# Optimization experiments

Hardware: AMD Instinct MI355X
Metric: run time of the kernel (lower is better)

## Reference

```python
import jax, jax.numpy as jnp
import numpy as np
from jax import lax

D_MODEL = 1024
SEQ_LEN = 8192
ORDER = 2
BATCH = 2

def setup_inputs() -> dict:
    key = jax.random.key(0)
    ks = jax.random.split(key, 16)
    s = 0.02
    return {
        'x': jax.random.normal(ks[0], (BATCH, SEQ_LEN, D_MODEL), jnp.float32),
        'in_proj_w': jax.random.normal(ks[1], (D_MODEL, D_MODEL * (ORDER + 1)), jnp.float32) * s,
        'in_proj_b': jax.random.normal(ks[2], (D_MODEL * (ORDER + 1),), jnp.float32) * s,
        'short_w': jax.random.normal(ks[3], (D_MODEL, 1, 3), jnp.float32) * 0.5,
        'short_b': jax.random.normal(ks[4], (D_MODEL,), jnp.float32) * s,
        'fw1': jax.random.normal(ks[5], (1, 64), jnp.float32) * 0.5,
        'fb1': jax.random.normal(ks[6], (64,), jnp.float32) * s,
        'fw2': jax.random.normal(ks[7], (64, 128), jnp.float32) * 0.1,
        'fb2': jax.random.normal(ks[8], (128,), jnp.float32) * s,
        'fw3': jax.random.normal(ks[9], (128, D_MODEL * ORDER), jnp.float32) * 0.05,
        'fb3': jax.random.normal(ks[10], (D_MODEL * ORDER,), jnp.float32) * s,
        'out_w': jax.random.normal(ks[11], (D_MODEL, D_MODEL), jnp.float32) * s,
        'out_b': jax.random.normal(ks[12], (D_MODEL,), jnp.float32) * s,
    }

def _hyena_fwd(x, in_proj_w, in_proj_b, short_w, short_b,
               fw1, fb1, fw2, fb2, fw3, fb3, out_w, out_b):
    B, L, C = x.shape
    # in_proj: (B, L, C*(order+1)) -> split into v and order gating branches
    proj = (x @ in_proj_w + in_proj_b).reshape(B, L, C, ORDER + 1)
    v = proj[..., 0]                                   # (B, L, C)
    x_branches = [proj[..., i] for i in range(1, ORDER + 1)]
    # depthwise short conv (kernel 3, same padding), torch Conv1d groups=C
    vc = v.transpose(0, 2, 1)                          # (B, C, L)
    vc = lax.conv_general_dilated(vc, short_w, window_strides=(1,),
                                  padding=((1, 1),), feature_group_count=C,
                                  dimension_numbers=('NCH', 'OIH', 'NCH'))
    v = (vc + short_b[None, :, None]).transpose(0, 2, 1)  # (B, L, C)
    # implicit filter: MLP over normalized positions (exact GELU as in torch)
    pos = jnp.linspace(0.0, 1.0, L, dtype=x.dtype)[:, None]   # (L, 1)
    h = jax.nn.gelu(pos @ fw1 + fb1, approximate=False)
    h = jax.nn.gelu(h @ fw2 + fb2, approximate=False)
    coefs = (h @ fw3 + fb3).reshape(L, C, ORDER)       # (L, C, order)
    # FFT long conv per order; v is constant across the loop (as in source)
    n = 2 * L
    v_fft = jnp.fft.rfft(v, n=n, axis=1)               # (B, L+1, C) complex
    output = v
    for i in range(ORDER):
        h_fft = jnp.fft.rfft(coefs[:, :, i], n=n, axis=0)   # (L+1, C)
        conv = jnp.fft.irfft(v_fft * h_fft[None], n=n, axis=1)[:, :L, :]
        output = x_branches[i] * conv                  # overwrites, as in source
    return output @ out_w + out_b                      # (B, L, C)

def reference(x, in_proj_w, in_proj_b, short_w, short_b,
              fw1, fb1, fw2, fb2, fw3, fb3, out_w, out_b):
    return _hyena_fwd(x, in_proj_w, in_proj_b, short_w, short_b,
                      fw1, fb1, fw2, fb2, fw3, fb3, out_w, out_b)
```

## Files before the change

kernel.cpp:

```cpp
#include <hip/hip_runtime.h>
#include <math.h>


constexpr int Lseq = 8192;
constexpr int Cd   = 1024;
constexpr int BL   = 16384;
constexpr int NF   = 16384;
constexpr int KK   = 1024;
constexpr int FT   = 1024;

constexpr size_t BIG_OFF  = 0;
constexpr size_t COEF_OFF = BIG_OFF + (size_t)2048 * BL;
constexpr size_t W2TH_OFF = COEF_OFF + (size_t)Cd * Lseq;
constexpr size_t W2TL_OFF = W2TH_OFF + (size_t)2048 * 1024 / 2;
constexpr size_t WOTH_OFF = W2TL_OFF + (size_t)2048 * 1024 / 2;
constexpr size_t WOTL_OFF = WOTH_OFF + (size_t)1024 * 1024 / 2;
constexpr size_t B2_OFF   = WOTL_OFF + (size_t)1024 * 1024 / 2;
constexpr size_t WS_FLOATS = B2_OFF + 2048;

using bf16x8 = __attribute__((ext_vector_type(8))) short;
using f32x4  = __attribute__((ext_vector_type(4))) float;

__device__ inline unsigned short f2bf(float f) {
  unsigned u = __float_as_uint(f);
  u += 0x7FFFu + ((u >> 16) & 1u);
  return (unsigned short)(u >> 16);
}
__device__ inline float bf2f(unsigned short h) { return __uint_as_float(((unsigned)h) << 16); }

__device__ inline void gload_lds16(const void* g, void* l) {
  __builtin_amdgcn_global_load_lds((const __attribute__((address_space(1))) unsigned int*)g,
                                   (__attribute__((address_space(3))) unsigned int*)l, 16, 0, 0);
}

__device__ inline float2 cadd(float2 a, float2 b){ return make_float2(a.x+b.x, a.y+b.y); }
__device__ inline float2 csub(float2 a, float2 b){ return make_float2(a.x-b.x, a.y-b.y); }
__device__ inline float2 cmul(float2 a, float2 b){ return make_float2(a.x*b.x - a.y*b.y, a.x*b.y + a.y*b.x); }
__device__ inline float2 cmulc(float2 a, float2 w){ return make_float2(a.x*w.x + a.y*w.y, a.y*w.x - a.x*w.y); }

__device__ inline int PD(int i) { return i + (i >> 4); }

__device__ inline float2 twW(int m) {
  float s, c;
  __sincosf((float)m * -3.8349519697141029e-4f, &s, &c);
  return make_float2(c, s);
}

__device__ inline void fftDIF(float2* __restrict__ z, int t) {
  for (int lq = 12; lq >= 0; lq -= 2) {
    int q    = 1 << lq;
    int twsh = 12 - lq;
    #pragma unroll
    for (int mb = 0; mb < 4; ++mb) {
      int m    = t + mb * FT;
      int tloc = m & (q - 1);
      int g    = m >> lq;
      int base = (g << (lq + 2)) + tloc;
      int i0 = PD(base), i1 = PD(base + q), i2 = PD(base + 2*q), i3 = PD(base + 3*q);
      float2 a = z[i0], b = z[i1], c = z[i2], d = z[i3];
      float2 t0 = cadd(a, c), t1 = csub(a, c);
      float2 t2 = cadd(b, d), t3 = csub(b, d);
      float2 y0 = cadd(t0, t2);
      float2 y2 = csub(t0, t2);
      float2 y1 = make_float2(t1.x + t3.y, t1.y - t3.x);
      float2 y3 = make_float2(t1.x - t3.y, t1.y + t3.x);
      int m1 = tloc << twsh;
      float2 w1 = twW(m1);
      float2 w2 = make_float2(w1.x*w1.x - w1.y*w1.y, 2.f*w1.x*w1.y);
      float2 w3 = cmul(w1, w2);
      z[i0] = y0;
      z[i1] = cmul(y1, w1);
      z[i2] = cmul(y2, w2);
      z[i3] = cmul(y3, w3);
    }
    __syncthreads();
  }
}

__device__ inline void fftDIT(float2* __restrict__ z, int t) {
  for (int lq = 0; lq <= 12; lq += 2) {
    int q    = 1 << lq;
    int twsh = 12 - lq;
    #pragma unroll
    for (int mb = 0; mb < 4; ++mb) {
      int m    = t + mb * FT;
      int tloc = m & (q - 1);
      int g    = m >> lq;
      int base = (g << (lq + 2)) + tloc;
      int i0 = PD(base), i1 = PD(base + q), i2 = PD(base + 2*q), i3 = PD(base + 3*q);
      int m1 = tloc << twsh;
      float2 w1 = twW(m1);
      float2 w2 = make_float2(w1.x*w1.x - w1.y*w1.y, 2.f*w1.x*w1.y);
      float2 w3 = cmul(w1, w2);
      float2 a = z[i0];
      float2 b = cmulc(z[i1], w1);
      float2 c = cmulc(z[i2], w2);
      float2 d = cmulc(z[i3], w3);
      float2 s0 = cadd(a, c), s1 = csub(a, c);
      float2 s2 = cadd(b, d), s3 = csub(b, d);
      z[i0] = cadd(s0, s2);
      z[i1] = make_float2(s1.x - s3.y, s1.y + s3.x);
      z[i2] = csub(s0, s2);
      z[i3] = make_float2(s1.x + s3.y, s1.y - s3.x);
    }
    __syncthreads();
  }
}

__global__ __launch_bounds__(256) void mlp_kernel(const float* __restrict__ fw1, const float* __restrict__ fb1,
                                                  const float* __restrict__ fw2, const float* __restrict__ fb2,
                                                  float* __restrict__ h2) {
  __shared__ float sw2[64 * 128];
  __shared__ float sw1[64], sb1[64], sb2[128];
  int t = threadIdx.x;
  for (int i = t; i < 64 * 128; i += 256) sw2[i] = fw2[i];
  if (t < 64)  { sw1[t] = fw1[t]; sb1[t] = fb1[t]; }
  if (t < 128) sb2[t] = fb2[t];
  __syncthreads();
  int l = blockIdx.x * 256 + t;
  float pos = (float)l / 8191.0f;
  float h1[64];
  #pragma unroll
  for (int j = 0; j < 64; ++j) {
    float xx = pos * sw1[j] + sb1[j];
    h1[j] = 0.5f * xx * (1.0f + erff(xx * 0.7071067811865475f));
  }
  for (int m = 0; m < 128; ++m) {
    float acc = sb2[m];
    #pragma unroll
    for (int j = 0; j < 64; ++j) acc += h1[j] * sw2[j * 128 + m];
    h2[(size_t)l * 128 + m] = 0.5f * acc * (1.0f + erff(acc * 0.7071067811865475f));
  }
}

__global__ __launch_bounds__(256) void gemm_coefs_kernel(const float* __restrict__ H2,
    const float* __restrict__ FW3, const float* __restrict__ FB3,
    float* __restrict__ coefs) {
  __shared__ float As[16 * 72];
  __shared__ float Bs[16 * 72];
  int t  = threadIdx.x;
  int n0 = blockIdx.x * 64;
  int m0 = blockIdx.y * 64;
  int tr = t >> 4, tc = t & 15;
  float acc[4][4] = {};
  int am = t >> 2, ak = (t & 3) * 4;
  int bk = t >> 4, bn = (t & 15) * 4;
  for (int k0 = 0; k0 < 128; k0 += 16) {
    float4 a = *(const float4*)&H2[(size_t)(m0 + am) * 128 + k0 + ak];
    float b0 = FW3[(size_t)(k0 + bk) * 2048 + 2 * (n0 + bn + 0) + 1];
    float b1 = FW3[(size_t)(k0 + bk) * 2048 + 2 * (n0 + bn + 1) + 1];
    float b2 = FW3[(size_t)(k0 + bk) * 2048 + 2 * (n0 + bn + 2) + 1];
    float b3 = FW3[(size_t)(k0 + bk) * 2048 + 2 * (n0 + bn + 3) + 1];
    __syncthreads();
    As[(ak + 0) * 72 + am] = a.x;
    As[(ak + 1) * 72 + am] = a.y;
    As[(ak + 2) * 72 + am] = a.z;
    As[(ak + 3) * 72 + am] = a.w;
    Bs[bk * 72 + bn + 0] = b0;
    Bs[bk * 72 + bn + 1] = b1;
    Bs[bk * 72 + bn + 2] = b2;
    Bs[bk * 72 + bn + 3] = b3;
    __syncthreads();
    #pragma unroll
    for (int kk = 0; kk < 16; ++kk) {
      float4 av = *(const float4*)&As[kk * 72 + tr * 4];
      float4 bv = *(const float4*)&Bs[kk * 72 + tc * 4];
      float aa[4] = {av.x, av.y, av.z, av.w};
      float bb[4] = {bv.x, bv.y, bv.z, bv.w};
      #pragma unroll
      for (int i = 0; i < 4; ++i)
        #pragma unroll
        for (int j = 0; j < 4; ++j)
          acc[i][j] += aa[i] * bb[j];
    }
  }
  #pragma unroll
  for (int j = 0; j < 4; ++j) {
    int c = n0 + tc * 4 + j;
    float bias = FB3[2 * c + 1];
    float4 val = make_float4(acc[0][j] + bias, acc[1][j] + bias, acc[2][j] + bias, acc[3][j] + bias);
    *(float4*)&coefs[(size_t)c * Lseq + m0 + tr * 4] = val;
  }
}

__global__ __launch_bounds__(256) void compact_w_kernel(const float* __restrict__ w, const float* __restrict__ b,
    unsigned short* __restrict__ w2h, unsigned short* __restrict__ w2l, float* __restrict__ b2) {
  __shared__ float t[64 * 65];
  int n0 = blockIdx.x * 64;
  int k0 = blockIdx.y * 64;
  int tid = threadIdx.x;
  #pragma unroll
  for (int i = 0; i < 16; ++i) {
    int idx = tid + i * 256;
    int nr = idx & 63, kr = idx >> 6;
    int n = n0 + nr;
    int src = (n < 1024) ? 3 * n : 3 * (n - 1024) + 2;
    t[nr * 65 + kr] = w[(size_t)(k0 + kr) * 3072 + src];
  }
  __syncthreads();
  #pragma unroll
  for (int i = 0; i < 16; ++i) {
    int idx = tid + i * 256;
    int kr = idx & 63, nr = idx >> 6;
    float v = t[nr * 65 + kr];
    unsigned short h = f2bf(v);
    size_t o = (size_t)(n0 + nr) * 1024 + k0 + kr;
    w2h[o] = h;
    w2l[o] = f2bf(v - bf2f(h));
  }
  if (blockIdx.y == 0 && tid < 64) {
    int n = n0 + tid;
    int src = (n < 1024) ? 3 * n : 3 * (n - 1024) + 2;
    b2[n] = b[src];
  }
}

__global__ __launch_bounds__(256) void wout_t_kernel(const float* __restrict__ w,
    unsigned short* __restrict__ wh, unsigned short* __restrict__ wl) {
  __shared__ float t[64 * 65];
  int n0 = blockIdx.x * 64, k0 = blockIdx.y * 64;
  int tid = threadIdx.x;
  #pragma unroll
  for (int i = 0; i < 16; ++i) {
    int idx = tid + i * 256;
    int nr = idx & 63, kr = idx >> 6;
    t[nr * 65 + kr] = w[(size_t)(k0 + kr) * 1024 + n0 + nr];
  }
  __syncthreads();
  #pragma unroll
  for (int i = 0; i < 16; ++i) {
    int idx = tid + i * 256;
    int kr = idx & 63, nr = idx >> 6;
    float v = t[nr * 65 + kr];
    unsigned short h = f2bf(v);
    size_t o = (size_t)(n0 + nr) * 1024 + k0 + kr;
    wh[o] = h;
    wl[o] = f2bf(v - bf2f(h));
  }
}

__global__ __launch_bounds__(256) void convert_x_kernel(const float* __restrict__ x,
    unsigned short* __restrict__ xhi, unsigned short* __restrict__ xlo) {
  size_t i = (size_t)blockIdx.x * 256 + threadIdx.x;
  size_t stride = (size_t)gridDim.x * 256;
  size_t n4 = (size_t)BL * 1024 / 4;
  for (; i < n4; i += stride) {
    float4 v = *(const float4*)&x[i * 4];
    ushort4 h, l;
    h.x = f2bf(v.x); l.x = f2bf(v.x - bf2f(h.x));
    h.y = f2bf(v.y); l.y = f2bf(v.y - bf2f(h.y));
    h.z = f2bf(v.z); l.z = f2bf(v.z - bf2f(h.z));
    h.w = f2bf(v.w); l.w = f2bf(v.w - bf2f(h.w));
    *(ushort4*)&xhi[i * 4] = h;
    *(ushort4*)&xlo[i * 4] = l;
  }
}

__global__ __launch_bounds__(256) void transpose_y_kernel(const float* __restrict__ y,
    unsigned short* __restrict__ yh, unsigned short* __restrict__ yl) {
  __shared__ float t[64 * 65];
  int m0 = blockIdx.x * 64, c0 = blockIdx.y * 64;
  int tid = threadIdx.x;
  #pragma unroll
  for (int i = 0; i < 16; ++i) {
    int idx = tid + i * 256;
    int mr = idx & 63, cr = idx >> 6;
    t[cr * 65 + mr] = y[(size_t)(c0 + cr) * BL + m0 + mr];
  }
  __syncthreads();
  #pragma unroll
  for (int i = 0; i < 16; ++i) {
    int idx = tid + i * 256;
    int cr = idx & 63, mr = idx >> 6;
    float v = t[cr * 65 + mr];
    unsigned short h = f2bf(v);
    size_t o = (size_t)(m0 + mr) * 1024 + c0 + cr;
    yh[o] = h;
    yl[o] = f2bf(v - bf2f(h));
  }
}

template<int BIAS_MODE>
__global__ __launch_bounds__(256) void gemm_bt_mfma(
    const unsigned short* __restrict__ Ahi, const unsigned short* __restrict__ Alo,
    const unsigned short* __restrict__ Bhi, const unsigned short* __restrict__ Blo,
    float* __restrict__ Cc, size_t ldc, const float* __restrict__ bias) {
  __shared__ unsigned short lds[4][128 * 32];
  int tid  = threadIdx.x;
  int lane = tid & 63;
  int wid  = tid >> 6;
  int wr = wid >> 1, wc = wid & 1;
  size_t row0 = (size_t)blockIdx.y * 128;
  size_t col0 = (size_t)blockIdx.x * 128;

  f32x4 acc[4][4];
  #pragma unroll
  for (int i = 0; i < 4; ++i)
    #pragma unroll
    for (int j = 0; j < 4; ++j) acc[i][j] = (f32x4){0.f, 0.f, 0.f, 0.f};

  const unsigned short* srcs[4] = {Ahi + row0 * KK, Alo + row0 * KK,
                                   Bhi + col0 * KK, Blo + col0 * KK};
  int ko = (lane >> 4) * 8;

  for (int k0 = 0; k0 < KK; k0 += 32) {
    #pragma unroll
    for (int t4 = 0; t4 < 4; ++t4) {
      const unsigned short* sp = srcs[t4] + k0;
      #pragma unroll
      for (int h = 0; h < 2; ++h) {
        int q = h * 256 + tid;
        int r = q >> 2, kp = (q & 3) * 8;
        gload_lds16(sp + (size_t)r * KK + kp, &lds[t4][q * 8]);
      }
    }
    __syncthreads();
    bf16x8 ah[4], al[4], bh[4], bl[4];
    #pragma unroll
    for (int f = 0; f < 4; ++f) {
      int ra = wr * 64 + f * 16 + (lane & 15);
      int rb = wc * 64 + f * 16 + (lane & 15);
      ah[f] = *(const bf16x8*)&lds[0][ra * 32 + ko];
      al[f] = *(const bf16x8*)&lds[1][ra * 32 + ko];
      bh[f] = *(const bf16x8*)&lds[2][rb * 32 + ko];
      bl[f] = *(const bf16x8*)&lds[3][rb * 32 + ko];
    }
    #pragma unroll
    for (int i = 0; i < 4; ++i)
      #pragma unroll
      for (int j = 0; j < 4; ++j) {
        acc[i][j] = __builtin_amdgcn_mfma_f32_16x16x32_bf16(ah[i], bh[j], acc[i][j], 0, 0, 0);
        acc[i][j] = __builtin_amdgcn_mfma_f32_16x16x32_bf16(ah[i], bl[j], acc[i][j], 0, 0, 0);
        acc[i][j] = __builtin_amdgcn_mfma_f32_16x16x32_bf16(al[i], bh[j], acc[i][j], 0, 0, 0);
      }
    __syncthreads();
  }

  #pragma unroll
  for (int i = 0; i < 4; ++i) {
    #pragma unroll
    for (int rr = 0; rr < 4; ++rr) {
      size_t row = row0 + wr * 64 + i * 16 + (lane >> 4) * 4 + rr;
      float rb = (BIAS_MODE == 0) ? bias[row] : 0.f;
      #pragma unroll
      for (int j = 0; j < 4; ++j) {
        size_t col = col0 + wc * 64 + j * 16 + (lane & 15);
        float cb = (BIAS_MODE == 1) ? bias[col] : rb;
        Cc[row * ldc + col] = acc[i][j][rr] + cb;
      }
    }
  }
}

__global__ __launch_bounds__(FT) void conv_fft_kernel(
    const float* __restrict__ vt, float* __restrict__ x2t,
    const float* __restrict__ coefs,
    const float* __restrict__ short_w, const float* __restrict__ short_b) {
  extern __shared__ float2 z[];
  int t = threadIdx.x;
  int c = blockIdx.x;

  const float* cf = coefs + (size_t)c * Lseq;
  for (int l = t; l < Lseq; l += FT)      z[PD(l)] = make_float2(cf[l], 0.f);
  for (int l = Lseq + t; l < NF; l += FT) z[PD(l)] = make_float2(0.f, 0.f);
  __syncthreads();
  fftDIF(z, t);

  float2 Hreg[16];
  constexpr float invN = 1.0f / (float)NF;
  #pragma unroll
  for (int j = 0; j < 16; ++j) {
    float2 h = z[PD(t + FT * j)];
    Hreg[j] = make_float2(h.x * invN, h.y * invN);
  }
  __syncthreads();

  float sw0 = short_w[c * 3 + 0], sw1 = short_w[c * 3 + 1], sw2 = short_w[c * 3 + 2];
  float sbv = short_b[c];
  const float* v0 = vt + (size_t)c * BL;
  const float* v1 = v0 + Lseq;
  for (int l = t; l < Lseq; l += FT) {
    float a0 = (l > 0)        ? v0[l - 1] : 0.f;
    float b0 = v0[l];
    float c0 = (l < Lseq - 1) ? v0[l + 1] : 0.f;
    float a1 = (l > 0)        ? v1[l - 1] : 0.f;
    float b1 = v1[l];
    float c1 = (l < Lseq - 1) ? v1[l + 1] : 0.f;
    z[PD(l)] = make_float2(sw0 * a0 + sw1 * b0 + sw2 * c0 + sbv,
                           sw0 * a1 + sw1 * b1 + sw2 * c1 + sbv);
  }
  for (int l = Lseq + t; l < NF; l += FT) z[PD(l)] = make_float2(0.f, 0.f);
  __syncthreads();
  fftDIF(z, t);

  #pragma unroll
  for (int j = 0; j < 16; ++j) {
    int p = PD(t + FT * j);
    z[p] = cmul(z[p], Hreg[j]);
  }
  __syncthreads();
  fftDIT(z, t);

  float* y0 = x2t + (size_t)c * BL;
  float* y1 = y0 + Lseq;
  for (int l = t; l < Lseq; l += FT) {
    float2 cv = z[PD(l)];
    y0[l] = y0[l] * cv.x;
    y1[l] = y1[l] * cv.y;
  }
}

extern "C" void kernel_launch(void* const* d_in, const int* in_sizes, int n_in,
                              void* d_out, int out_size, void* d_ws, size_t ws_size,
                              hipStream_t stream) {
  (void)in_sizes; (void)n_in; (void)out_size;
  const float* x    = (const float*)d_in[0];
  const float* ipw  = (const float*)d_in[1];
  const float* ipb  = (const float*)d_in[2];
  const float* sw   = (const float*)d_in[3];
  const float* sb   = (const float*)d_in[4];
  const float* fw1  = (const float*)d_in[5];
  const float* fb1  = (const float*)d_in[6];
  const float* fw2  = (const float*)d_in[7];
  const float* fb2  = (const float*)d_in[8];
  const float* fw3  = (const float*)d_in[9];
  const float* fb3  = (const float*)d_in[10];
  const float* outw = (const float*)d_in[11];
  const float* outb = (const float*)d_in[12];
  float* out = (float*)d_out;
  float* ws  = (float*)d_ws;

  if (ws_size < WS_FLOATS * 4) return;

  float*          big   = ws + BIG_OFF;
  float*          vt    = big;
  float*          x2t   = big + (size_t)Cd * BL;
  float*          coefs = ws + COEF_OFF;
  unsigned short* w2h   = (unsigned short*)(ws + W2TH_OFF);
  unsigned short* w2l   = (unsigned short*)(ws + W2TL_OFF);
  unsigned short* woh   = (unsigned short*)(ws + WOTH_OFF);
  unsigned short* wol   = (unsigned short*)(ws + WOTL_OFF);
  float*          b2    = ws + B2_OFF;
  float*          h2    = ws + W2TH_OFF;
  unsigned short* xhi   = (unsigned short*)d_out;
  unsigned short* xlo   = xhi + (size_t)BL * 1024;
  unsigned short* yhi   = (unsigned short*)big;
  unsigned short* ylo   = yhi + (size_t)BL * 1024;

  constexpr int CONV_LDS = 17408 * 8;
  hipFuncSetAttribute(reinterpret_cast<const void*>(conv_fft_kernel),
                      hipFuncAttributeMaxDynamicSharedMemorySize, CONV_LDS);

  mlp_kernel<<<32, 256, 0, stream>>>(fw1, fb1, fw2, fb2, h2);
  gemm_coefs_kernel<<<dim3(16, 128), 256, 0, stream>>>(h2, fw3, fb3, coefs);
  compact_w_kernel<<<dim3(32, 16), 256, 0, stream>>>(ipw, ipb, w2h, w2l, b2);
  wout_t_kernel<<<dim3(16, 16), 256, 0, stream>>>(outw, woh, wol);
  convert_x_kernel<<<2048, 256, 0, stream>>>(x, xhi, xlo);
  gemm_bt_mfma<0><<<dim3(128, 16), 256, 0, stream>>>(w2h, w2l, xhi, xlo, big, (size_t)BL, b2);
  conv_fft_kernel<<<1024, FT, CONV_LDS, stream>>>(vt, x2t, coefs, sw, sb);
  transpose_y_kernel<<<dim3(256, 16), 256, 0, stream>>>(x2t, yhi, ylo);
  gemm_bt_mfma<1><<<dim3(8, 128), 256, 0, stream>>>(yhi, ylo, woh, wol, out, (size_t)1024, outb);
}
```

Measured before the change: 778.9 us.

## Restructure FFT conv into register-resident radix-16 phases with fewer LDS passes

Replaces the seven-stage LDS-based radix-4 FFT, which synchronises after every stage, with a four-pass scheme. Each thread keeps 16 complex values in registers and performs two radix-4 stages per pass. The first pass consumes the global loads directly and the last inverse pass writes output from registers. The final forward radix-4 stage, the pointwise multiply and the first inverse stage are fused into one pass. This removes many LDS round trips and barriers, at the cost of higher register pressure, and the launch_bounds hint could force spills.

```diff
diff --git a/kernel.cpp b/kernel.cpp
--- a/kernel.cpp
+++ b/kernel.cpp
@@ -7,7 +7,6 @@
 constexpr int BL   = 16384;
 constexpr int NF   = 16384;
 constexpr int KK   = 1024;
-constexpr int FT   = 1024;
 
 constexpr size_t BIG_OFF  = 0;
 constexpr size_t COEF_OFF = BIG_OFF + (size_t)2048 * BL;
@@ -40,70 +39,117 @@
 
 __device__ inline int PD(int i) { return i + (i >> 4); }
 
-__device__ inline float2 twW(int m) {
+__device__ inline void tw3(int m1, float2& w1, float2& w2, float2& w3) {
   float s, c;
-  __sincosf((float)m * -3.8349519697141029e-4f, &s, &c);
-  return make_float2(c, s);
-}
-
-__device__ inline void fftDIF(float2* __restrict__ z, int t) {
-  for (int lq = 12; lq >= 0; lq -= 2) {
-    int q    = 1 << lq;
-    int twsh = 12 - lq;
-    #pragma unroll
-    for (int mb = 0; mb < 4; ++mb) {
-      int m    = t + mb * FT;
-      int tloc = m & (q - 1);
-      int g    = m >> lq;
-      int base = (g << (lq + 2)) + tloc;
-      int i0 = PD(base), i1 = PD(base + q), i2 = PD(base + 2*q), i3 = PD(base + 3*q);
-      float2 a = z[i0], b = z[i1], c = z[i2], d = z[i3];
-      float2 t0 = cadd(a, c), t1 = csub(a, c);
-      float2 t2 = cadd(b, d), t3 = csub(b, d);
-      float2 y0 = cadd(t0, t2);
-      float2 y2 = csub(t0, t2);
-      float2 y1 = make_float2(t1.x + t3.y, t1.y - t3.x);
-      float2 y3 = make_float2(t1.x - t3.y, t1.y + t3.x);
-      int m1 = tloc << twsh;
-      float2 w1 = twW(m1);
-      float2 w2 = make_float2(w1.x*w1.x - w1.y*w1.y, 2.f*w1.x*w1.y);
-      float2 w3 = cmul(w1, w2);
-      z[i0] = y0;
-      z[i1] = cmul(y1, w1);
-      z[i2] = cmul(y2, w2);
-      z[i3] = cmul(y3, w3);
-    }
-    __syncthreads();
-  }
-}
-
-__device__ inline void fftDIT(float2* __restrict__ z, int t) {
-  for (int lq = 0; lq <= 12; lq += 2) {
-    int q    = 1 << lq;
-    int twsh = 12 - lq;
-    #pragma unroll
-    for (int mb = 0; mb < 4; ++mb) {
-      int m    = t + mb * FT;
-      int tloc = m & (q - 1);
-      int g    = m >> lq;
-      int base = (g << (lq + 2)) + tloc;
-      int i0 = PD(base), i1 = PD(base + q), i2 = PD(base + 2*q), i3 = PD(base + 3*q);
-      int m1 = tloc << twsh;
-      float2 w1 = twW(m1);
-      float2 w2 = make_float2(w1.x*w1.x - w1.y*w1.y, 2.f*w1.x*w1.y);
-      float2 w3 = cmul(w1, w2);
-      float2 a = z[i0];
-      float2 b = cmulc(z[i1], w1);
-      float2 c = cmulc(z[i2], w2);
-      float2 d = cmulc(z[i3], w3);
-      float2 s0 = cadd(a, c), s1 = csub(a, c);
-      float2 s2 = cadd(b, d), s3 = csub(b, d);
-      z[i0] = cadd(s0, s2);
-      z[i1] = make_float2(s1.x - s3.y, s1.y + s3.x);
-      z[i2] = csub(s0, s2);
-      z[i3] = make_float2(s1.x + s3.y, s1.y - s3.x);
-    }
-    __syncthreads();
+  __sincosf((float)m1 * -3.8349519697141029e-4f, &s, &c);
+  w1 = make_float2(c, s);
+  w2 = make_float2(c*c - s*s, 2.f*c*s);
+  w3 = cmul(w1, w2);
+}
+
+__device__ inline void bfly4_fwd(float2& A, float2& B, float2& C, float2& D,
+                                 float2 w1, float2 w2, float2 w3) {
+  float2 t0 = cadd(A, C), t1 = csub(A, C);
+  float2 t2 = cadd(B, D), t3 = csub(B, D);
+  float2 y0 = cadd(t0, t2), y2 = csub(t0, t2);
+  float2 y1 = make_float2(t1.x + t3.y, t1.y - t3.x);
+  float2 y3 = make_float2(t1.x - t3.y, t1.y + t3.x);
+  A = y0; B = cmul(y1, w1); C = cmul(y2, w2); D = cmul(y3, w3);
+}
+__device__ inline void bfly4_fwd_nt(float2& A, float2& B, float2& C, float2& D) {
+  float2 t0 = cadd(A, C), t1 = csub(A, C);
+  float2 t2 = cadd(B, D), t3 = csub(B, D);
+  float2 y1 = make_float2(t1.x + t3.y, t1.y - t3.x);
+  float2 y3 = make_float2(t1.x - t3.y, t1.y + t3.x);
+  A = cadd(t0, t2); C = csub(t0, t2); B = y1; D = y3;
+}
+__device__ inline void bfly4_inv(float2& A, float2& B, float2& C, float2& D,
+                                 float2 w1, float2 w2, float2 w3) {
+  float2 b = cmulc(B, w1), c = cmulc(C, w2), e = cmulc(D, w3);
+  float2 s0 = cadd(A, c), s1 = csub(A, c);
+  float2 s2 = cadd(b, e), s3 = csub(b, e);
+  A = cadd(s0, s2); C = csub(s0, s2);
+  B = make_float2(s1.x - s3.y, s1.y + s3.x);
+  D = make_float2(s1.x + s3.y, s1.y - s3.x);
+}
+__device__ inline void bfly4_inv_nt(float2& A, float2& B, float2& C, float2& D) {
+  float2 s0 = cadd(A, C), s1 = csub(A, C);
+  float2 s2 = cadd(B, D), s3 = csub(B, D);
+  A = cadd(s0, s2); C = csub(s0, s2);
+  B = make_float2(s1.x - s3.y, s1.y + s3.x);
+  D = make_float2(s1.x + s3.y, s1.y - s3.x);
+}
+
+__device__ inline void phaseA_fwd(float2 (&d)[16], int t) {
+  float2 w1, w2, w3;
+  #pragma unroll
+  for (int j0 = 0; j0 < 4; ++j0) {
+    tw3(t + 1024*j0, w1, w2, w3);
+    bfly4_fwd(d[j0], d[j0+4], d[j0+8], d[j0+12], w1, w2, w3);
+  }
+  tw3(4*t, w1, w2, w3);
+  #pragma unroll
+  for (int a = 0; a < 4; ++a)
+    bfly4_fwd(d[4*a], d[4*a+1], d[4*a+2], d[4*a+3], w1, w2, w3);
+}
+__device__ inline void phaseA_inv(float2 (&d)[16], int t) {
+  float2 w1, w2, w3;
+  tw3(4*t, w1, w2, w3);
+  #pragma unroll
+  for (int a = 0; a < 4; ++a)
+    bfly4_inv(d[4*a], d[4*a+1], d[4*a+2], d[4*a+3], w1, w2, w3);
+  #pragma unroll
+  for (int j0 = 0; j0 < 4; ++j0) {
+    tw3(t + 1024*j0, w1, w2, w3);
+    bfly4_inv(d[j0], d[j0+4], d[j0+8], d[j0+12], w1, w2, w3);
+  }
+}
+__device__ inline void phaseB_fwd(float2 (&d)[16], int r) {
+  float2 w1, w2, w3;
+  #pragma unroll
+  for (int j0 = 0; j0 < 4; ++j0) {
+    tw3((r + 64*j0) << 4, w1, w2, w3);
+    bfly4_fwd(d[j0], d[j0+4], d[j0+8], d[j0+12], w1, w2, w3);
+  }
+  tw3(r << 6, w1, w2, w3);
+  #pragma unroll
+  for (int a = 0; a < 4; ++a)
+    bfly4_fwd(d[4*a], d[4*a+1], d[4*a+2], d[4*a+3], w1, w2, w3);
+}
+__device__ inline void phaseB_inv(float2 (&d)[16], int r) {
+  float2 w1, w2, w3;
+  tw3(r << 6, w1, w2, w3);
+  #pragma unroll
+  for (int a = 0; a < 4; ++a)
+    bfly4_inv(d[4*a], d[4*a+1], d[4*a+2], d[4*a+3], w1, w2, w3);
+  #pragma unroll
+  for (int j0 = 0; j0 < 4; ++j0) {
+    tw3((r + 64*j0) << 4, w1, w2, w3);
+    bfly4_inv(d[j0], d[j0+4], d[j0+8], d[j0+12], w1, w2, w3);
+  }
+}
+__device__ inline void phaseC_fwd(float2 (&d)[16], int u) {
+  float2 w1, w2, w3;
+  #pragma unroll
+  for (int j0 = 0; j0 < 4; ++j0) {
+    tw3((u + 4*j0) << 8, w1, w2, w3);
+    bfly4_fwd(d[j0], d[j0+4], d[j0+8], d[j0+12], w1, w2, w3);
+  }
+  tw3(u << 10, w1, w2, w3);
+  #pragma unroll
+  for (int a = 0; a < 4; ++a)
+    bfly4_fwd(d[4*a], d[4*a+1], d[4*a+2], d[4*a+3], w1, w2, w3);
+}
+__device__ inline void phaseC_inv(float2 (&d)[16], int u) {
+  float2 w1, w2, w3;
+  tw3(u << 10, w1, w2, w3);
+  #pragma unroll
+  for (int a = 0; a < 4; ++a)
+    bfly4_inv(d[4*a], d[4*a+1], d[4*a+2], d[4*a+3], w1, w2, w3);
+  #pragma unroll
+  for (int j0 = 0; j0 < 4; ++j0) {
+    tw3((u + 4*j0) << 8, w1, w2, w3);
+    bfly4_inv(d[j0], d[j0+4], d[j0+8], d[j0+12], w1, w2, w3);
   }
 }
 
@@ -352,61 +398,136 @@
   }
 }
 
-__global__ __launch_bounds__(FT) void conv_fft_kernel(
+__global__ __launch_bounds__(1024, 4) void conv_fft_kernel(
     const float* __restrict__ vt, float* __restrict__ x2t,
     const float* __restrict__ coefs,
     const float* __restrict__ short_w, const float* __restrict__ short_b) {
   extern __shared__ float2 z[];
   int t = threadIdx.x;
   int c = blockIdx.x;
-
-  const float* cf = coefs + (size_t)c * Lseq;
-  for (int l = t; l < Lseq; l += FT)      z[PD(l)] = make_float2(cf[l], 0.f);
-  for (int l = Lseq + t; l < NF; l += FT) z[PD(l)] = make_float2(0.f, 0.f);
-  __syncthreads();
-  fftDIF(z, t);
-
+  int rB = t & 63;
+  int baseB = (t >> 6) * 1024 + rB;
+  int u = t & 3;
+  int baseC = (t >> 2) * 64 + u;
+
+  float2 d[16];
   float2 Hreg[16];
   constexpr float invN = 1.0f / (float)NF;
-  #pragma unroll
-  for (int j = 0; j < 16; ++j) {
-    float2 h = z[PD(t + FT * j)];
-    Hreg[j] = make_float2(h.x * invN, h.y * invN);
-  }
-  __syncthreads();
-
-  float sw0 = short_w[c * 3 + 0], sw1 = short_w[c * 3 + 1], sw2 = short_w[c * 3 + 2];
-  float sbv = short_b[c];
-  const float* v0 = vt + (size_t)c * BL;
-  const float* v1 = v0 + Lseq;
-  for (int l = t; l < Lseq; l += FT) {
-    float a0 = (l > 0)        ? v0[l - 1] : 0.f;
-    float b0 = v0[l];
-    float c0 = (l < Lseq - 1) ? v0[l + 1] : 0.f;
-    float a1 = (l > 0)        ? v1[l - 1] : 0.f;
-    float b1 = v1[l];
-    float c1 = (l < Lseq - 1) ? v1[l + 1] : 0.f;
-    z[PD(l)] = make_float2(sw0 * a0 + sw1 * b0 + sw2 * c0 + sbv,
-                           sw0 * a1 + sw1 * b1 + sw2 * c1 + sbv);
-  }
-  for (int l = Lseq + t; l < NF; l += FT) z[PD(l)] = make_float2(0.f, 0.f);
-  __syncthreads();
-  fftDIF(z, t);
-
-  #pragma unroll
-  for (int j = 0; j < 16; ++j) {
-    int p = PD(t + FT * j);
-    z[p] = cmul(z[p], Hreg[j]);
-  }
-  __syncthreads();
-  fftDIT(z, t);
-
-  float* y0 = x2t + (size_t)c * BL;
-  float* y1 = y0 + Lseq;
-  for (int l = t; l < Lseq; l += FT) {
-    float2 cv = z[PD(l)];
-    y0[l] = y0[l] * cv.x;
-    y1[l] = y1[l] * cv.y;
+
+  {
+    const float* cf = coefs + (size_t)c * Lseq;
+    #pragma unroll
+    for (int j = 0; j < 8; ++j)  d[j] = make_float2(cf[t + 1024 * j], 0.f);
+    #pragma unroll
+    for (int j = 8; j < 16; ++j) d[j] = make_float2(0.f, 0.f);
+    phaseA_fwd(d, t);
+    #pragma unroll
+    for (int j = 0; j < 16; ++j) z[PD(t + 1024 * j)] = d[j];
+    __syncthreads();
+
+    #pragma unroll
+    for (int j = 0; j < 16; ++j) d[j] = z[PD(baseB + 64 * j)];
+    phaseB_fwd(d, rB);
+    #pragma unroll
+    for (int j = 0; j < 16; ++j) z[PD(baseB + 64 * j)] = d[j];
+    __syncthreads();
+
+    #pragma unroll
+    for (int j = 0; j < 16; ++j) d[j] = z[PD(baseC + 4 * j)];
+    phaseC_fwd(d, u);
+    #pragma unroll
+    for (int j = 0; j < 16; ++j) z[PD(baseC + 4 * j)] = d[j];
+    __syncthreads();
+
+    #pragma unroll
+    for (int s = 0; s < 4; ++s) {
+      int ib = 17 * t + 4 * s;
+      float2 A = z[ib], B = z[ib + 1], C = z[ib + 2], D = z[ib + 3];
+      bfly4_fwd_nt(A, B, C, D);
+      Hreg[4*s+0] = make_float2(A.x * invN, A.y * invN);
+      Hreg[4*s+1] = make_float2(B.x * invN, B.y * invN);
+      Hreg[4*s+2] = make_float2(C.x * invN, C.y * invN);
+      Hreg[4*s+3] = make_float2(D.x * invN, D.y * invN);
+    }
+    __syncthreads();
+  }
+
+  {
+    float sw0 = short_w[c * 3 + 0], sw1 = short_w[c * 3 + 1], sw2 = short_w[c * 3 + 2];
+    float sbv = short_b[c];
+    const float* v0 = vt + (size_t)c * BL;
+    const float* v1 = v0 + Lseq;
+    #pragma unroll
+    for (int j = 0; j < 8; ++j) {
+      int l = t + 1024 * j;
+      float a0 = (l > 0)        ? v0[l - 1] : 0.f;
+      float b0 = v0[l];
+      float c0 = (l < Lseq - 1) ? v0[l + 1] : 0.f;
+      float a1 = (l > 0)        ? v1[l - 1] : 0.f;
+      float b1 = v1[l];
+      float c1 = (l < Lseq - 1) ? v1[l + 1] : 0.f;
+      d[j] = make_float2(sw0 * a0 + sw1 * b0 + sw2 * c0 + sbv,
+                         sw0 * a1 + sw1 * b1 + sw2 * c1 + sbv);
+    }
+    #pragma unroll
+    for (int j = 8; j < 16; ++j) d[j] = make_float2(0.f, 0.f);
+    phaseA_fwd(d, t);
+    #pragma unroll
+    for (int j = 0; j < 16; ++j) z[PD(t + 1024 * j)] = d[j];
+    __syncthreads();
+
+    #pragma unroll
+    for (int j = 0; j < 16; ++j) d[j] = z[PD(baseB + 64 * j)];
+    phaseB_fwd(d, rB);
+    #pragma unroll
+    for (int j = 0; j < 16; ++j) z[PD(baseB + 64 * j)] = d[j];
+    __syncthreads();
+
+    #pragma unroll
+    for (int j = 0; j < 16; ++j) d[j] = z[PD(baseC + 4 * j)];
+    phaseC_fwd(d, u);
+    #pragma unroll
+    for (int j = 0; j < 16; ++j) z[PD(baseC + 4 * j)] = d[j];
+    __syncthreads();
+
+    #pragma unroll
+    for (int s = 0; s < 4; ++s) {
+      int ib = 17 * t + 4 * s;
+      float2 A = z[ib], B = z[ib + 1], C = z[ib + 2], D = z[ib + 3];
+      bfly4_fwd_nt(A, B, C, D);
+      A = cmul(A, Hreg[4*s+0]); B = cmul(B, Hreg[4*s+1]);
+      C = cmul(C, Hreg[4*s+2]); D = cmul(D, Hreg[4*s+3]);
+      bfly4_inv_nt(A, B, C, D);
+      z[ib] = A; z[ib + 1] = B; z[ib + 2] = C; z[ib + 3] = D;
+    }
+    __syncthreads();
+
+    #pragma unroll
+    for (int j = 0; j < 16; ++j) d[j] = z[PD(baseC + 4 * j)];
+    phaseC_inv(d, u);
+    #pragma unroll
+    for (int j = 0; j < 16; ++j) z[PD(baseC + 4 * j)] = d[j];
+    __syncthreads();
+
+    #pragma unroll
+    for (int j = 0; j < 16; ++j) d[j] = z[PD(baseB + 64 * j)];
+    phaseB_inv(d, rB);
+    #pragma unroll
+    for (int j = 0; j < 16; ++j) z[PD(baseB + 64 * j)] = d[j];
+    __syncthreads();
+
+    #pragma unroll
+    for (int j = 0; j < 16; ++j) d[j] = z[PD(t + 1024 * j)];
+    phaseA_inv(d, t);
+
+    float* y0 = x2t + (size_t)c * BL;
+    float* y1 = y0 + Lseq;
+    #pragma unroll
+    for (int j = 0; j < 8; ++j) {
+      int l = t + 1024 * j;
+      y0[l] = y0[l] * d[j].x;
+      y1[l] = y1[l] * d[j].y;
+    }
   }
 }
 
@@ -457,7 +578,7 @@
   wout_t_kernel<<<dim3(16, 16), 256, 0, stream>>>(outw, woh, wol);
   convert_x_kernel<<<2048, 256, 0, stream>>>(x, xhi, xlo);
   gemm_bt_mfma<0><<<dim3(128, 16), 256, 0, stream>>>(w2h, w2l, xhi, xlo, big, (size_t)BL, b2);
-  conv_fft_kernel<<<1024, FT, CONV_LDS, stream>>>(vt, x2t, coefs, sw, sb);
+  conv_fft_kernel<<<1024, 1024, CONV_LDS, stream>>>(vt, x2t, coefs, sw, sb);
   transpose_y_kernel<<<dim3(256, 16), 256, 0, stream>>>(x2t, yhi, ylo);
   gemm_bt_mfma<1><<<dim3(8, 128), 256, 0, stream>>>(yhi, ylo, woh, wol, out, (size_t)1024, outb);
 }
```

Result: slower. 1.154 ms (+48.2%).
